# Kernel tuning notes

Hardware: AMD Instinct MI355X
Metric: run time of the kernel (lower is better)

## Reference

```python
import jax, jax.numpy as jnp
import numpy as np

N, K = 50000, 10      # nodes, sampled neighbors (num_sample)
V, F = 200000, 128    # embedding table rows, input_dim
H = 64                # hidden per direction (hidden_dim=128, bidirectional)


def setup_inputs() -> dict:
    key = jax.random.key(0)
    ks = jax.random.split(key, 12)
    s = 1.0 / np.sqrt(H)  # torch LSTM init: U(-1/sqrt(H), 1/sqrt(H))
    u = lambda k, shape: jax.random.uniform(k, shape, jnp.float32, -s, s)
    return {
        "neigh_idx": jax.random.randint(ks[0], (N, K), 0, V),
        "embed_table": jax.random.normal(ks[1], (V, F), jnp.float32) * 0.02,
        # forward-direction LSTM params (torch gate order: i, f, g, o)
        "Wih_f": u(ks[2], (4 * H, F)), "Whh_f": u(ks[3], (4 * H, H)),
        "bih_f": u(ks[4], (4 * H,)),   "bhh_f": u(ks[5], (4 * H,)),
        # backward-direction LSTM params
        "Wih_b": u(ks[6], (4 * H, F)), "Whh_b": u(ks[7], (4 * H, H)),
        "bih_b": u(ks[8], (4 * H,)),   "bhh_b": u(ks[9], (4 * H,)),
    }


def _lstm_scan(x, Wih, Whh, bih, bhh):
    """x: [N,K,F] -> hidden outputs [N,K,H] (single direction)."""
    n = x.shape[0]
    # precompute input projections for all steps: [N,K,4H]
    xg = jnp.einsum('nkf,gf->nkg', x, Wih) + bih + bhh
    h0 = jnp.zeros((n, H), x.dtype)
    c0 = jnp.zeros((n, H), x.dtype)

    def step(carry, xt):
        h, c = carry
        gates = xt + h @ Whh.T
        i, f, g, o = jnp.split(gates, 4, axis=-1)
        i = jax.nn.sigmoid(i)
        f = jax.nn.sigmoid(f)
        g = jnp.tanh(g)
        o = jax.nn.sigmoid(o)
        c = f * c + i * g
        h = o * jnp.tanh(c)
        return (h, c), h

    _, hs = jax.lax.scan(step, (h0, c0), jnp.swapaxes(xg, 0, 1))  # [K,N,H]
    return jnp.swapaxes(hs, 0, 1)


def reference(neigh_idx, embed_table, Wih_f, Whh_f, bih_f, bhh_f,
              Wih_b, Whh_b, bih_b, bhh_b):
    x = embed_table[neigh_idx]  # gather: [N,K,F]
    # forward direction: last-step hidden
    h_f = _lstm_scan(x, Wih_f, Whh_f, bih_f, bhh_f)[:, -1, :]
    # backward direction processes reversed sequence; torch output[:, -1] of the
    # backward stream is its hidden after processing only element K-1 (step 0).
    h_b = _lstm_scan(x[:, ::-1, :], Wih_b, Whh_b, bih_b, bhh_b)[:, 0, :]
    return jnp.concatenate([h_f, h_b], axis=-1)  # [N, 2H]
```

## Files before the change

kernel.cpp:

```cpp
#include <hip/hip_runtime.h>
#include <hip/hip_bf16.h>


#define NN 50000
#define KK 10
#define FF 128
#define HH 64

#define WS_WIH_F 0
#define WS_WHH_F 32768
#define WS_WIH_B 49152

#define NPB 32
#define NT 1563
#define GRID 512
#define HS 72

typedef __bf16 bf16x8 __attribute__((ext_vector_type(8)));
typedef float f32x4 __attribute__((ext_vector_type(4)));
typedef float f32x2 __attribute__((ext_vector_type(2)));

#if __has_builtin(__builtin_amdgcn_exp2f)
#define EXP2(x) __builtin_amdgcn_exp2f(x)
#else
#define EXP2(x) exp2f(x)
#endif

__device__ __forceinline__ float fast_sig(float x) {
    float e = EXP2(x * -1.44269504f);
    return __builtin_amdgcn_rcpf(1.0f + e);
}
__device__ __forceinline__ float fast_tanh(float x) {
    float e = EXP2(x * 2.88539008f);
    return 1.0f - 2.0f * __builtin_amdgcn_rcpf(e + 1.0f);
}
__device__ __forceinline__ f32x2 sig2(f32x2 x) {
    f32x2 t = x * -1.44269504f;
    f32x2 e = {EXP2(t.x), EXP2(t.y)};
    f32x2 d = e + 1.0f;
    return (f32x2){__builtin_amdgcn_rcpf(d.x), __builtin_amdgcn_rcpf(d.y)};
}
__device__ __forceinline__ f32x2 tanh2(f32x2 x) {
    f32x2 t = x * 2.88539008f;
    f32x2 e = {EXP2(t.x), EXP2(t.y)};
    f32x2 d = e + 1.0f;
    f32x2 r = {__builtin_amdgcn_rcpf(d.x), __builtin_amdgcn_rcpf(d.y)};
    return 1.0f - 2.0f * r;
}

__global__ void cvt_weights_kernel(const float* __restrict__ Wih_f,
                                   const float* __restrict__ Whh_f,
                                   const float* __restrict__ Wih_b,
                                   __bf16* __restrict__ ws) {
    int i = blockIdx.x * 256 + threadIdx.x;
    ws[WS_WIH_F + i] = (__bf16)Wih_f[i];
    if (i < 16384) ws[WS_WHH_F + i] = (__bf16)Whh_f[i];
    ws[WS_WIH_B + i] = (__bf16)Wih_b[i];
}

#define STAGE_LOAD(Gs, kidx)                                                  \
    do {                                                                      \
        const float* _src = tab + (size_t)gq[srow][(kidx)] * FF + spart * 16; \
        _Pragma("unroll")                                                     \
        for (int _j = 0; _j < 4; ++_j) Gs[_j] = *(const f32x4*)(_src + _j * 4);\
    } while (0)

#define STAGE_WRITE(Gs, b)                                                    \
    do {                                                                      \
        bf16x8 _v0, _v1;                                                      \
        _Pragma("unroll")                                                     \
        for (int _e = 0; _e < 4; ++_e) {                                      \
            _v0[_e]     = (__bf16)Gs[0][_e];                                  \
            _v0[4 + _e] = (__bf16)Gs[1][_e];                                  \
            _v1[_e]     = (__bf16)Gs[2][_e];                                  \
            _v1[4 + _e] = (__bf16)Gs[3][_e];                                  \
        }                                                                     \
        char* _row = (char*)(x_lds[(b)] + srow * FF);                         \
        *(bf16x8*)(_row + ((spart * 32)      ^ swW)) = _v0;                   \
        *(bf16x8*)(_row + ((spart * 32 + 16) ^ swW)) = _v1;                   \
    } while (0)

#define STEP_BARRIER()                                                        \
    do {                                                                      \
        asm volatile("s_waitcnt lgkmcnt(0)" ::: "memory");                    \
        __builtin_amdgcn_s_barrier();                                         \
        __builtin_amdgcn_sched_barrier(0);                                    \
    } while (0)

__global__ __launch_bounds__(256, 2) void lstm_agg_kernel(
    const int* __restrict__ nidx,
    const float* __restrict__ tab,
    const float* __restrict__ bih_f,
    const float* __restrict__ bhh_f,
    const float* __restrict__ bih_b,
    const float* __restrict__ bhh_b,
    const __bf16* __restrict__ ws,
    float* __restrict__ out)
{
    __shared__ __bf16 x_lds[2][NPB * FF];
    __shared__ __bf16 h_lds[2][NPB * HS];
    __shared__ int    gq[NPB][KK];

    const int tid  = threadIdx.x;
    const int w    = tid >> 6;
    const int lane = tid & 63;
    const int q    = lane >> 4;
    const int c    = lane & 15;
    const int koff = q * 8;
    const int sw = (c & 7) << 4;

    const int srow  = tid >> 3;
    const int spart = tid & 7;
    const int swW   = (srow & 7) << 4;

    f32x4 GA[4], GB[4];

    bf16x8 bWih[4][4], bWhh[4][2];
#pragma unroll
    for (int g = 0; g < 4; ++g) {
        int row = (g * 4 + w) * 16 + c;
#pragma unroll
        for (int kk = 0; kk < 4; ++kk)
            bWih[g][kk] = *(const bf16x8*)(ws + WS_WIH_F + row * FF + kk * 32 + koff);
#pragma unroll
        for (int kk = 0; kk < 2; ++kk)
            bWhh[g][kk] = *(const bf16x8*)(ws + WS_WHH_F + row * HH + kk * 32 + koff);
    }
    float bias[4];
#pragma unroll
    for (int g = 0; g < 4; ++g) {
        int u = g * 64 + w * 16 + c;
        bias[g] = bih_f[u] + bhh_f[u];
    }

    for (int tile = blockIdx.x; tile < NT; tile += GRID) {
        const int node_base = tile * NPB;

        __syncthreads();
        for (int i = tid; i < NPB * KK; i += 256) {
            int r = i / KK, k = i - r * KK;
            int node = min(node_base + r, NN - 1);
            gq[r][k] = nidx[node * KK + k];
        }
        __syncthreads();

        STAGE_LOAD(GA, 0);
        STAGE_LOAD(GB, 1);
        __builtin_amdgcn_sched_barrier(0);
        STAGE_WRITE(GA, 0);
        STEP_BARRIER();

        f32x4 acc[4][2];
        float cst[2][4];
#pragma unroll
        for (int r = 0; r < 2; ++r)
#pragma unroll
            for (int e = 0; e < 4; ++e) cst[r][e] = 0.0f;

#pragma unroll 2
        for (int k = 0; k < KK; ++k) {
            const int cur = k & 1;
            if (k + 2 < KK) {
                if ((k & 1) == 0) STAGE_LOAD(GA, k + 2);
                else              STAGE_LOAD(GB, k + 2);
                __builtin_amdgcn_sched_barrier(0);
            }

#pragma unroll
            for (int g = 0; g < 4; ++g)
#pragma unroll
                for (int r = 0; r < 2; ++r)
                    acc[g][r] = (f32x4){bias[g], bias[g], bias[g], bias[g]};

            __builtin_amdgcn_s_setprio(1);
            const char* xb = (const char*)x_lds[cur];
#pragma unroll
            for (int r = 0; r < 2; ++r) {
                const char* rp = xb + (r * 16 + c) * 256;
                bf16x8 xa[4];
#pragma unroll
                for (int kk = 0; kk < 4; ++kk)
                    xa[kk] = *(const bf16x8*)(rp + ((kk * 64 + q * 16) ^ sw));
#pragma unroll
                for (int g = 0; g < 4; ++g)
#pragma unroll
                    for (int kk = 0; kk < 4; ++kk)
                        acc[g][r] = __builtin_amdgcn_mfma_f32_16x16x32_bf16(
                            xa[kk], bWih[g][kk], acc[g][r], 0, 0, 0);
            }
            if (k > 0) {
                const __bf16* hb = h_lds[(k - 1) & 1];
#pragma unroll
                for (int r = 0; r < 2; ++r) {
                    bf16x8 ha[2];
#pragma unroll
                    for (int kk = 0; kk < 2; ++kk)
                        ha[kk] = *(const bf16x8*)(hb + (r * 16 + c) * HS + kk * 32 + koff);
#pragma unroll
                    for (int g = 0; g < 4; ++g)
#pragma unroll
                        for (int kk = 0; kk < 2; ++kk)
                            acc[g][r] = __builtin_amdgcn_mfma_f32_16x16x32_bf16(
                                ha[kk], bWhh[g][kk], acc[g][r], 0, 0, 0);
                }
            }
            __builtin_amdgcn_s_setprio(0);

            const bool last = (k == KK - 1);
            __bf16* hw = h_lds[k & 1];
#pragma unroll
            for (int r = 0; r < 2; ++r)
#pragma unroll
                for (int p = 0; p < 2; ++p) {
                    f32x2 ai = {acc[0][r][2 * p], acc[0][r][2 * p + 1]};
                    f32x2 af = {acc[1][r][2 * p], acc[1][r][2 * p + 1]};
                    f32x2 ag = {acc[2][r][2 * p], acc[2][r][2 * p + 1]};
                    f32x2 ao = {acc[3][r][2 * p], acc[3][r][2 * p + 1]};
                    f32x2 gi = sig2(ai);
                    f32x2 gf = sig2(af);
                    f32x2 gg = tanh2(ag);
                    f32x2 go = sig2(ao);
                    f32x2 cc = {cst[r][2 * p], cst[r][2 * p + 1]};
                    f32x2 cn = gf * cc + gi * gg;
                    cst[r][2 * p]     = cn.x;
                    cst[r][2 * p + 1] = cn.y;
                    f32x2 h = go * tanh2(cn);
                    hw[(r * 16 + q * 4 + 2 * p)     * HS + w * 16 + c] = (__bf16)h.x;
                    hw[(r * 16 + q * 4 + 2 * p + 1) * HS + w * 16 + c] = (__bf16)h.y;
                    if (last) {
                        int node = node_base + r * 16 + q * 4 + 2 * p;
                        if (node < NN)     out[(size_t)node * 128 + w * 16 + c] = h.x;
                        if (node + 1 < NN) out[(size_t)(node + 1) * 128 + w * 16 + c] = h.y;
                    }
                }

            if (k + 1 < KK) {
                if (((k + 1) & 1) == 0) STAGE_WRITE(GA, 0);
                else                    STAGE_WRITE(GB, 1);
            }
            STEP_BARRIER();
        }

        {
            const int gb[3] = {0, 2, 3};
            const char* xb = (const char*)x_lds[(KK - 1) & 1];
            f32x4 ab[3][2];
#pragma unroll
            for (int j = 0; j < 3; ++j) {
                int row = (gb[j] * 4 + w) * 16 + c;
                bf16x8 bW[4];
#pragma unroll
                for (int kk = 0; kk < 4; ++kk)
                    bW[kk] = *(const bf16x8*)(ws + WS_WIH_B + row * FF + kk * 32 + koff);
                int u = gb[j] * 64 + w * 16 + c;
                float bb = bih_b[u] + bhh_b[u];
#pragma unroll
                for (int r = 0; r < 2; ++r) {
                    f32x4 a = (f32x4){bb, bb, bb, bb};
                    const char* rp = xb + (r * 16 + c) * 256;
#pragma unroll
                    for (int kk = 0; kk < 4; ++kk) {
                        bf16x8 xa = *(const bf16x8*)(rp + ((kk * 64 + q * 16) ^ sw));
                        a = __builtin_amdgcn_mfma_f32_16x16x32_bf16(xa, bW[kk], a, 0, 0, 0);
                    }
                    ab[j][r] = a;
                }
            }
#pragma unroll
            for (int r = 0; r < 2; ++r)
#pragma unroll
                for (int reg = 0; reg < 4; ++reg) {
                    float gi = fast_sig(ab[0][r][reg]);
                    float gg = fast_tanh(ab[1][r][reg]);
                    float go = fast_sig(ab[2][r][reg]);
                    float hb2 = go * fast_tanh(gi * gg);
                    int node = node_base + r * 16 + q * 4 + reg;
                    if (node < NN) out[(size_t)node * 128 + 64 + w * 16 + c] = hb2;
                }
        }
    }
}

extern "C" void kernel_launch(void* const* d_in, const int* in_sizes, int n_in,
                              void* d_out, int out_size, void* d_ws, size_t ws_size,
                              hipStream_t stream) {
    const int*   nidx  = (const int*)d_in[0];
    const float* tab   = (const float*)d_in[1];
    const float* Wih_f = (const float*)d_in[2];
    const float* Whh_f = (const float*)d_in[3];
    const float* bih_f = (const float*)d_in[4];
    const float* bhh_f = (const float*)d_in[5];
    const float* Wih_b = (const float*)d_in[6];
    const float* bih_b = (const float*)d_in[8];
    const float* bhh_b = (const float*)d_in[9];
    __bf16* ws  = (__bf16*)d_ws;
    float*  out = (float*)d_out;

    hipLaunchKernelGGL(cvt_weights_kernel, dim3(32768 / 256), dim3(256), 0, stream,
                       Wih_f, Whh_f, Wih_b, ws);

    hipLaunchKernelGGL(lstm_agg_kernel, dim3(GRID), dim3(256), 0, stream,
                       nidx, tab, bih_f, bhh_f, bih_b, bhh_b, ws, out);
}
```

Before: 228.6 us.

## Software-pipeline input projection across steps and split tail into half tiles

```diff
diff --git a/kernel.cpp b/kernel.cpp
--- a/kernel.cpp
+++ b/kernel.cpp
@@ -12,8 +12,10 @@
 #define WS_WIH_B 49152
 
 #define NPB 32
-#define NT 1563
+#define NTB 1536
 #define GRID 512
+#define TAIL_NODE0 49152
+#define TAIL_BLOCKS 53
 #define HS 72
 
 typedef __bf16 bf16x8 __attribute__((ext_vector_type(8)));
@@ -87,6 +89,184 @@
         __builtin_amdgcn_sched_barrier(0);                                    \
     } while (0)
 
+template<int R>
+__device__ __forceinline__ void lstm_tile(
+    int node_base, int tid, int w, int q, int c, int koff, int sw,
+    int srow, int spart, int swW,
+    const int* __restrict__ nidx, const float* __restrict__ tab,
+    const __bf16* __restrict__ ws,
+    const float* __restrict__ bih_b, const float* __restrict__ bhh_b,
+    const bf16x8 (&bWih)[4][4], const bf16x8 (&bWhh)[4][2],
+    const float (&bias)[4],
+    __bf16 (*x_lds)[NPB * FF], __bf16 (*h_lds)[NPB * HS], int (*gq)[KK],
+    float* __restrict__ out)
+{
+    __syncthreads();
+    for (int i = tid; i < R * 16 * KK; i += 256) {
+        int r = i / KK, k = i - r * KK;
+        int node = min(node_base + r, NN - 1);
+        gq[r][k] = nidx[node * KK + k];
+    }
+    __syncthreads();
+
+    const bool sact = (srow < R * 16);
+    f32x4 GA[4];
+    {
+        f32x4 GB[4];
+        if (sact) { STAGE_LOAD(GA, 0); STAGE_LOAD(GB, 1); }
+        __builtin_amdgcn_sched_barrier(0);
+        if (sact) { STAGE_WRITE(GA, 0); STAGE_WRITE(GB, 1); }
+    }
+    STEP_BARRIER();
+
+    f32x4 acc[2][4][2];
+    float cst[2][4];
+#pragma unroll
+    for (int r = 0; r < R; ++r)
+#pragma unroll
+        for (int e = 0; e < 4; ++e) cst[r][e] = 0.0f;
+
+#pragma unroll
+    for (int g = 0; g < 4; ++g)
+#pragma unroll
+        for (int r = 0; r < R; ++r)
+            acc[0][g][r] = (f32x4){bias[g], bias[g], bias[g], bias[g]};
+    {
+        const char* xb = (const char*)x_lds[0];
+#pragma unroll
+        for (int r = 0; r < R; ++r) {
+            const char* rp = xb + (r * 16 + c) * 256;
+            bf16x8 xa[4];
+#pragma unroll
+            for (int kk = 0; kk < 4; ++kk)
+                xa[kk] = *(const bf16x8*)(rp + ((kk * 64 + q * 16) ^ sw));
+#pragma unroll
+            for (int g = 0; g < 4; ++g)
+#pragma unroll
+                for (int kk = 0; kk < 4; ++kk)
+                    acc[0][g][r] = __builtin_amdgcn_mfma_f32_16x16x32_bf16(
+                        xa[kk], bWih[g][kk], acc[0][g][r], 0, 0, 0);
+        }
+    }
+
+#pragma unroll 2
+    for (int k = 0; k < KK; ++k) {
+        const int pa = k & 1, pb = (k + 1) & 1;
+        if (k + 2 < KK && sact) STAGE_LOAD(GA, k + 2);
+        __builtin_amdgcn_sched_barrier(0);
+
+        __builtin_amdgcn_s_setprio(1);
+        if (k > 0) {
+            const __bf16* hb = h_lds[pb];
+#pragma unroll
+            for (int r = 0; r < R; ++r) {
+                bf16x8 ha[2];
+#pragma unroll
+                for (int kk = 0; kk < 2; ++kk)
+                    ha[kk] = *(const bf16x8*)(hb + (r * 16 + c) * HS + kk * 32 + koff);
+#pragma unroll
+                for (int g = 0; g < 4; ++g)
+#pragma unroll
+                    for (int kk = 0; kk < 2; ++kk)
+                        acc[pa][g][r] = __builtin_amdgcn_mfma_f32_16x16x32_bf16(
+                            ha[kk], bWhh[g][kk], acc[pa][g][r], 0, 0, 0);
+            }
+        }
+        if (k + 1 < KK) {
+#pragma unroll
+            for (int g = 0; g < 4; ++g)
+#pragma unroll
+                for (int r = 0; r < R; ++r)
+                    acc[pb][g][r] = (f32x4){bias[g], bias[g], bias[g], bias[g]};
+            const char* xb = (const char*)x_lds[pb];
+#pragma unroll
+            for (int r = 0; r < R; ++r) {
+                const char* rp = xb + (r * 16 + c) * 256;
+                bf16x8 xa[4];
+#pragma unroll
+                for (int kk = 0; kk < 4; ++kk)
+                    xa[kk] = *(const bf16x8*)(rp + ((kk * 64 + q * 16) ^ sw));
+#pragma unroll
+                for (int g = 0; g < 4; ++g)
+#pragma unroll
+                    for (int kk = 0; kk < 4; ++kk)
+                        acc[pb][g][r] = __builtin_amdgcn_mfma_f32_16x16x32_bf16(
+                            xa[kk], bWih[g][kk], acc[pb][g][r], 0, 0, 0);
+            }
+        }
+        __builtin_amdgcn_s_setprio(0);
+
+        const bool last = (k == KK - 1);
+        __bf16* hw = h_lds[pa];
+#pragma unroll
+        for (int r = 0; r < R; ++r)
+#pragma unroll
+            for (int p = 0; p < 2; ++p) {
+                f32x2 ai = {acc[pa][0][r][2 * p], acc[pa][0][r][2 * p + 1]};
+                f32x2 af = {acc[pa][1][r][2 * p], acc[pa][1][r][2 * p + 1]};
+                f32x2 ag = {acc[pa][2][r][2 * p], acc[pa][2][r][2 * p + 1]};
+                f32x2 ao = {acc[pa][3][r][2 * p], acc[pa][3][r][2 * p + 1]};
+                f32x2 gi = sig2(ai);
+                f32x2 gf = sig2(af);
+                f32x2 gg = tanh2(ag);
+                f32x2 go = sig2(ao);
+                f32x2 cc = {cst[r][2 * p], cst[r][2 * p + 1]};
+                f32x2 cn = gf * cc + gi * gg;
+                cst[r][2 * p]     = cn.x;
+                cst[r][2 * p + 1] = cn.y;
+                f32x2 h = go * tanh2(cn);
+                hw[(r * 16 + q * 4 + 2 * p)     * HS + w * 16 + c] = (__bf16)h.x;
+                hw[(r * 16 + q * 4 + 2 * p + 1) * HS + w * 16 + c] = (__bf16)h.y;
+                if (last) {
+                    int node = node_base + r * 16 + q * 4 + 2 * p;
+                    if (node < NN)     out[(size_t)node * 128 + w * 16 + c] = h.x;
+                    if (node + 1 < NN) out[(size_t)(node + 1) * 128 + w * 16 + c] = h.y;
+                }
+            }
+
+        if (k + 2 < KK && sact) STAGE_WRITE(GA, pa);
+        STEP_BARRIER();
+    }
+
+    {
+        const int gb[3] = {0, 2, 3};
+        const char* xb = (const char*)x_lds[1];
+        f32x4 ab[3][2];
+#pragma unroll
+        for (int j = 0; j < 3; ++j) {
+            int row = (gb[j] * 4 + w) * 16 + c;
+            bf16x8 bW[4];
+#pragma unroll
+            for (int kk = 0; kk < 4; ++kk)
+                bW[kk] = *(const bf16x8*)(ws + WS_WIH_B + row * FF + kk * 32 + koff);
+            int u = gb[j] * 64 + w * 16 + c;
+            float bb = bih_b[u] + bhh_b[u];
+#pragma unroll
+            for (int r = 0; r < R; ++r) {
+                f32x4 a = (f32x4){bb, bb, bb, bb};
+                const char* rp = xb + (r * 16 + c) * 256;
+#pragma unroll
+                for (int kk = 0; kk < 4; ++kk) {
+                    bf16x8 xa = *(const bf16x8*)(rp + ((kk * 64 + q * 16) ^ sw));
+                    a = __builtin_amdgcn_mfma_f32_16x16x32_bf16(xa, bW[kk], a, 0, 0, 0);
+                }
+                ab[j][r] = a;
+            }
+        }
+#pragma unroll
+        for (int r = 0; r < R; ++r)
+#pragma unroll
+            for (int reg = 0; reg < 4; ++reg) {
+                float gi = fast_sig(ab[0][r][reg]);
+                float gg = fast_tanh(ab[1][r][reg]);
+                float go = fast_sig(ab[2][r][reg]);
+                float hb2 = go * fast_tanh(gi * gg);
+                int node = node_base + r * 16 + q * 4 + reg;
+                if (node < NN) out[(size_t)node * 128 + 64 + w * 16 + c] = hb2;
+            }
+    }
+}
+
 __global__ __launch_bounds__(256, 2) void lstm_agg_kernel(
     const int* __restrict__ nidx,
     const float* __restrict__ tab,
@@ -107,14 +287,12 @@
     const int q    = lane >> 4;
     const int c    = lane & 15;
     const int koff = q * 8;
-    const int sw = (c & 7) << 4;
+    const int sw   = (c & 7) << 4;
 
     const int srow  = tid >> 3;
     const int spart = tid & 7;
     const int swW   = (srow & 7) << 4;
 
-    f32x4 GA[4], GB[4];
-
     bf16x8 bWih[4][4], bWhh[4][2];
 #pragma unroll
     for (int g = 0; g < 4; ++g) {
@@ -133,152 +311,16 @@
         bias[g] = bih_f[u] + bhh_f[u];
     }
 
-    for (int tile = blockIdx.x; tile < NT; tile += GRID) {
-        const int node_base = tile * NPB;
-
-        __syncthreads();
-        for (int i = tid; i < NPB * KK; i += 256) {
-            int r = i / KK, k = i - r * KK;
-            int node = min(node_base + r, NN - 1);
-            gq[r][k] = nidx[node * KK + k];
-        }
-        __syncthreads();
-
-        STAGE_LOAD(GA, 0);
-        STAGE_LOAD(GB, 1);
-        __builtin_amdgcn_sched_barrier(0);
-        STAGE_WRITE(GA, 0);
-        STEP_BARRIER();
-
-        f32x4 acc[4][2];
-        float cst[2][4];
-#pragma unroll
-        for (int r = 0; r < 2; ++r)
-#pragma unroll
-            for (int e = 0; e < 4; ++e) cst[r][e] = 0.0f;
-
-#pragma unroll 2
-        for (int k = 0; k < KK; ++k) {
-            const int cur = k & 1;
-            if (k + 2 < KK) {
-                if ((k & 1) == 0) STAGE_LOAD(GA, k + 2);
-                else              STAGE_LOAD(GB, k + 2);
-                __builtin_amdgcn_sched_barrier(0);
-            }
-
-#pragma unroll
-            for (int g = 0; g < 4; ++g)
-#pragma unroll
-                for (int r = 0; r < 2; ++r)
-                    acc[g][r] = (f32x4){bias[g], bias[g], bias[g], bias[g]};
-
-            __builtin_amdgcn_s_setprio(1);
-            const char* xb = (const char*)x_lds[cur];
-#pragma unroll
-            for (int r = 0; r < 2; ++r) {
-                const char* rp = xb + (r * 16 + c) * 256;
-                bf16x8 xa[4];
-#pragma unroll
-                for (int kk = 0; kk < 4; ++kk)
-                    xa[kk] = *(const bf16x8*)(rp + ((kk * 64 + q * 16) ^ sw));
-#pragma unroll
-                for (int g = 0; g < 4; ++g)
-#pragma unroll
-                    for (int kk = 0; kk < 4; ++kk)
-                        acc[g][r] = __builtin_amdgcn_mfma_f32_16x16x32_bf16(
-                            xa[kk], bWih[g][kk], acc[g][r], 0, 0, 0);
-            }
-            if (k > 0) {
-                const __bf16* hb = h_lds[(k - 1) & 1];
-#pragma unroll
-                for (int r = 0; r < 2; ++r) {
-                    bf16x8 ha[2];
-#pragma unroll
-                    for (int kk = 0; kk < 2; ++kk)
-                        ha[kk] = *(const bf16x8*)(hb + (r * 16 + c) * HS + kk * 32 + koff);
-#pragma unroll
-                    for (int g = 0; g < 4; ++g)
-#pragma unroll
-                        for (int kk = 0; kk < 2; ++kk)
-                            acc[g][r] = __builtin_amdgcn_mfma_f32_16x16x32_bf16(
-                                ha[kk], bWhh[g][kk], acc[g][r], 0, 0, 0);
-                }
-            }
-            __builtin_amdgcn_s_setprio(0);
-
-            const bool last = (k == KK - 1);
-            __bf16* hw = h_lds[k & 1];
-#pragma unroll
-            for (int r = 0; r < 2; ++r)
-#pragma unroll
-                for (int p = 0; p < 2; ++p) {
-                    f32x2 ai = {acc[0][r][2 * p], acc[0][r][2 * p + 1]};
-                    f32x2 af = {acc[1][r][2 * p], acc[1][r][2 * p + 1]};
-                    f32x2 ag = {acc[2][r][2 * p], acc[2][r][2 * p + 1]};
-                    f32x2 ao = {acc[3][r][2 * p], acc[3][r][2 * p + 1]};
-                    f32x2 gi = sig2(ai);
-                    f32x2 gf = sig2(af);
-                    f32x2 gg = tanh2(ag);
-                    f32x2 go = sig2(ao);
-                    f32x2 cc = {cst[r][2 * p], cst[r][2 * p + 1]};
-                    f32x2 cn = gf * cc + gi * gg;
-                    cst[r][2 * p]     = cn.x;
-                    cst[r][2 * p + 1] = cn.y;
-                    f32x2 h = go * tanh2(cn);
-                    hw[(r * 16 + q * 4 + 2 * p)     * HS + w * 16 + c] = (__bf16)h.x;
-                    hw[(r * 16 + q * 4 + 2 * p + 1) * HS + w * 16 + c] = (__bf16)h.y;
-                    if (last) {
-                        int node = node_base + r * 16 + q * 4 + 2 * p;
-                        if (node < NN)     out[(size_t)node * 128 + w * 16 + c] = h.x;
-                        if (node + 1 < NN) out[(size_t)(node + 1) * 128 + w * 16 + c] = h.y;
-                    }
-                }
-
-            if (k + 1 < KK) {
-                if (((k + 1) & 1) == 0) STAGE_WRITE(GA, 0);
-                else                    STAGE_WRITE(GB, 1);
-            }
-            STEP_BARRIER();
-        }
-
-        {
-            const int gb[3] = {0, 2, 3};
-            const char* xb = (const char*)x_lds[(KK - 1) & 1];
-            f32x4 ab[3][2];
-#pragma unroll
-            for (int j = 0; j < 3; ++j) {
-                int row = (gb[j] * 4 + w) * 16 + c;
-                bf16x8 bW[4];
-#pragma unroll
-                for (int kk = 0; kk < 4; ++kk)
-                    bW[kk] = *(const bf16x8*)(ws + WS_WIH_B + row * FF + kk * 32 + koff);
-                int u = gb[j] * 64 + w * 16 + c;
-                float bb = bih_b[u] + bhh_b[u];
-#pragma unroll
-                for (int r = 0; r < 2; ++r) {
-                    f32x4 a = (f32x4){bb, bb, bb, bb};
-                    const char* rp = xb + (r * 16 + c) * 256;
-#pragma unroll
-                    for (int kk = 0; kk < 4; ++kk) {
-                        bf16x8 xa = *(const bf16x8*)(rp + ((kk * 64 + q * 16) ^ sw));
-                        a = __builtin_amdgcn_mfma_f32_16x16x32_bf16(xa, bW[kk], a, 0, 0, 0);
-                    }
-                    ab[j][r] = a;
-                }
-            }
-#pragma unroll
-            for (int r = 0; r < 2; ++r)
-#pragma unroll
-                for (int reg = 0; reg < 4; ++reg) {
-                    float gi = fast_sig(ab[0][r][reg]);
-                    float gg = fast_tanh(ab[1][r][reg]);
-                    float go = fast_sig(ab[2][r][reg]);
-                    float hb2 = go * fast_tanh(gi * gg);
-                    int node = node_base + r * 16 + q * 4 + reg;
-                    if (node < NN) out[(size_t)node * 128 + 64 + w * 16 + c] = hb2;
-                }
-        }
-    }
+    for (int t = blockIdx.x; t < NTB; t += GRID)
+        lstm_tile<2>(t * NPB, tid, w, q, c, koff, sw, srow, spart, swW,
+                     nidx, tab, ws, bih_b, bhh_b, bWih, bWhh, bias,
+                     x_lds, h_lds, gq, out);
+
+    if (blockIdx.x < TAIL_BLOCKS)
+        lstm_tile<1>(TAIL_NODE0 + (int)blockIdx.x * 16, tid, w, q, c, koff, sw,
+                     srow, spart, swW,
+                     nidx, tab, ws, bih_b, bhh_b, bWih, bWhh, bias,
+                     x_lds, h_lds, gq, out);
 }
 
 extern "C" void kernel_launch(void* const* d_in, const int* in_sizes, int n_in,
```

Result: slower. 237.0 us (+3.7%).
